# Performance work log

Hardware: AMD Instinct MI355X
Metric: run time of the kernel (lower is better)

Reference implementation:

```python
import jax, jax.numpy as jnp
import numpy as np

VS = VT = 32000; E = 512; H = 512; B = 32; S = 128; T = 128


def _gru_step(x, h, Wx, bx, Urz, brz, Un, bn):
    # x: [B, I], h: [B, H]
    gx = x @ Wx + bx                       # [B, 3H]
    xr, xz, xn = jnp.split(gx, 3, axis=-1)
    hrz = h @ Urz + brz                    # [B, 2H]
    hr, hz = jnp.split(hrz, 2, axis=-1)
    r = jax.nn.sigmoid(xr + hr)
    z = jax.nn.sigmoid(xz + hz)
    n = jnp.tanh(xn + (r * h) @ Un + bn)
    return (1.0 - z) * h + z * n


def setup_inputs() -> dict:
    key = jax.random.key(0)
    ks = jax.random.split(key, 24)
    s = 0.02
    f = lambda k, shape: (jax.random.normal(k, shape, dtype=jnp.float32) * s)
    return {
        "src": jax.random.randint(ks[0], (B, S), 0, VS),
        "tgt": jax.random.randint(ks[1], (B, T), 0, VT),
        "enc_embed": f(ks[2], (VS, E)),
        "enc_Wx": f(ks[3], (E, 3 * H)),
        "enc_bx": jnp.zeros((3 * H,), jnp.float32),
        "enc_Urz": f(ks[4], (H, 2 * H)),
        "enc_brz": jnp.zeros((2 * H,), jnp.float32),
        "enc_Un": f(ks[5], (H, H)),
        "enc_bn": jnp.zeros((H,), jnp.float32),
        "dec_embed": f(ks[6], (VT, E)),
        "dec_Wx": f(ks[7], (E + H, 3 * H)),
        "dec_bx": jnp.zeros((3 * H,), jnp.float32),
        "dec_Urz": f(ks[8], (H, 2 * H)),
        "dec_brz": jnp.zeros((2 * H,), jnp.float32),
        "dec_Un": f(ks[9], (H, H)),
        "dec_bn": jnp.zeros((H,), jnp.float32),
        "attn_Wh": f(ks[10], (H, H)),
        "attn_Ws": f(ks[11], (H, H)),
        "attn_v": f(ks[12], (H,)),
        "out_W": f(ks[13], (2 * H, VT)),
        "out_b": jnp.zeros((VT,), jnp.float32),
    }


def reference(src, tgt, enc_embed, enc_Wx, enc_bx, enc_Urz, enc_brz, enc_Un,
              enc_bn, dec_embed, dec_Wx, dec_bx, dec_Urz, dec_brz, dec_Un,
              dec_bn, attn_Wh, attn_Ws, attn_v, out_W, out_b):
    bs = src.shape[0]
    h0 = jnp.zeros((bs, H), dtype=enc_Wx.dtype)

    # -------- encoder: scan over src timesteps --------
    src_emb = enc_embed[src]                     # [B, S, E]

    def enc_step(h, x_t):
        h = _gru_step(x_t, h, enc_Wx, enc_bx, enc_Urz, enc_brz, enc_Un, enc_bn)
        return h, h

    h, enc_hs = jax.lax.scan(enc_step, h0, jnp.swapaxes(src_emb, 0, 1))
    enc_hs = jnp.swapaxes(enc_hs, 0, 1)          # [B, S, H]

    # precompute Wh(enc_hs), identical every decoder step
    wh_enc = enc_hs @ attn_Wh                    # [B, S, H]

    # -------- decoder: scan over tgt timesteps --------
    tgt_emb = dec_embed[tgt]                     # [B, T, E]

    def dec_step(h, emb_t):
        # Bahdanau attention
        energy = jnp.einsum('bsh,h->bs', jnp.tanh(wh_enc + (h @ attn_Ws)[:, None, :]), attn_v)
        attn = jax.nn.softmax(energy, axis=-1)   # [B, S]
        ctx = jnp.einsum('bs,bsh->bh', attn, enc_hs)
        x = jnp.concatenate([emb_t, ctx], axis=-1)   # [B, E+H]
        h = _gru_step(x, h, dec_Wx, dec_bx, dec_Urz, dec_brz, dec_Un, dec_bn)
        logits = jnp.concatenate([h, ctx], axis=-1) @ out_W + out_b
        out = jax.nn.log_softmax(logits, axis=-1)
        return h, out

    _, outputs = jax.lax.scan(dec_step, h, jnp.swapaxes(tgt_emb, 0, 1))
    return jnp.swapaxes(outputs, 0, 1)           # [B, T, VT]
```

## Files before the change

kernel.cpp:

```cpp
#include <hip/hip_runtime.h>
#include <stdint.h>

#define BATCH 32
#define SEQ   128
#define HID   512
#define VTOK  32000

typedef unsigned short u16;
typedef unsigned int   u32;
typedef unsigned long long u64;
typedef float    f32x4  __attribute__((ext_vector_type(4)));
typedef short    short8 __attribute__((ext_vector_type(8)));

__device__ __forceinline__ u16 f2bf(float f) {
    u32 u = __builtin_bit_cast(u32, f);
    return (u16)((u + 0x7FFFu + ((u >> 16) & 1u)) >> 16);
}
__device__ __forceinline__ float bf2f(u16 v) {
    u32 u = ((u32)v) << 16; return __builtin_bit_cast(float, u);
}
__device__ __forceinline__ float fexp2(float x) { return __builtin_amdgcn_exp2f(x); }
__device__ __forceinline__ float frcp(float x)  { return __builtin_amdgcn_rcpf(x); }
__device__ __forceinline__ float sigmoid_f(float x) {
    return frcp(1.f + fexp2(-1.442695040888963f * x));
}
__device__ __forceinline__ float tanh_f(float x) {
    return 1.f - 2.f * frcp(1.f + fexp2(2.885390081777927f * x));
}

__device__ __forceinline__ u32 ld_sc1_u32(const u32* p) {
    return __hip_atomic_load(p, __ATOMIC_RELAXED, __HIP_MEMORY_SCOPE_AGENT);
}
__device__ __forceinline__ void st_sc1_u32(u32* p, u32 v) {
    __hip_atomic_store(p, v, __ATOMIC_RELAXED, __HIP_MEMORY_SCOPE_AGENT);
}
__device__ __forceinline__ u64 ld_sc1_u64(const u64* p) {
    return __hip_atomic_load(p, __ATOMIC_RELAXED, __HIP_MEMORY_SCOPE_AGENT);
}
__device__ __forceinline__ short8 ldA(const u64* base) {
    union { u64 q[2]; short8 s; } u;
    u.q[0] = ld_sc1_u64(base);
    u.q[1] = ld_sc1_u64(base + 1);
    return u.s;
}

__device__ __forceinline__ void poll_ge(const u32* f, int idx, u32 gen) {
    const u32* p = f + (u32)idx * 16;
    while (ld_sc1_u32(p) < gen) {}
}
__device__ __forceinline__ void bump(u32* f, u32 gen) {
    asm volatile("s_waitcnt vmcnt(0)" ::: "memory");
    __syncthreads();
    if (threadIdx.x == 0) st_sc1_u32(f + (u32)blockIdx.x * 16, gen);
}


__global__ __launch_bounds__(256) void transpose_cvt(
    const float* __restrict__ src, u16* __restrict__ dst, int K, int N)
{
    __shared__ float tile[32][33];
    const int n0 = blockIdx.x * 32, k0 = blockIdx.y * 32;
    const int tx = threadIdx.x & 31, ty = threadIdx.x >> 5;
    #pragma unroll
    for (int j = 0; j < 32; j += 8)
        tile[ty + j][tx] = src[(size_t)(k0 + ty + j) * N + n0 + tx];
    __syncthreads();
    #pragma unroll
    for (int j = 0; j < 32; j += 8)
        dst[(size_t)(n0 + ty + j) * K + k0 + tx] = f2bf(tile[tx][ty + j]);
}

__global__ __launch_bounds__(256) void cvt_f32_bf16(
    const float* __restrict__ src, u16* __restrict__ dst)
{
    const size_t i = ((size_t)blockIdx.x * 256 + threadIdx.x) * 8;
    float4 v0 = *(const float4*)(src + i);
    float4 v1 = *(const float4*)(src + i + 4);
    uint4 pk;
    pk.x = (u32)f2bf(v0.x) | ((u32)f2bf(v0.y) << 16);
    pk.y = (u32)f2bf(v0.z) | ((u32)f2bf(v0.w) << 16);
    pk.z = (u32)f2bf(v1.x) | ((u32)f2bf(v1.y) << 16);
    pk.w = (u32)f2bf(v1.z) | ((u32)f2bf(v1.w) << 16);
    *(uint4*)(dst + i) = pk;
}

__global__ __launch_bounds__(128) void gather_emb_bf16(
    const int* __restrict__ idx, const float* __restrict__ emb, u16* __restrict__ out)
{
    const int r = blockIdx.x;
    const int token = idx[r];
    const int i = threadIdx.x * 4;
    float4 v = *(const float4*)(emb + (size_t)token * 512 + i);
    uint2 pk;
    pk.x = (u32)f2bf(v.x) | ((u32)f2bf(v.y) << 16);
    pk.y = (u32)f2bf(v.z) | ((u32)f2bf(v.w) << 16);
    *(uint2*)(out + (size_t)r * 512 + i) = pk;
}

__global__ __launch_bounds__(512) void init_state(u32* hg, u32* bar)
{
    const int i = blockIdx.x * 512 + threadIdx.x;
    hg[i] = 0u;
    if (blockIdx.x < 6) bar[blockIdx.x * 512 + threadIdx.x] = 0u;
}

__global__ __launch_bounds__(256) void gemm_bf16(
    const u16* __restrict__ A, const u16* __restrict__ BT,
    const float* __restrict__ bias, float* __restrict__ C,
    int M, int N, int K)
{
    __shared__ __align__(16) u16 As[128][40];
    __shared__ __align__(16) u16 Bs[128][40];
    const int tid  = threadIdx.x;
    const int lane = tid & 63, wave = tid >> 6;
    const int wm = (wave & 1) * 64, wn = (wave >> 1) * 64;
    const int lrow = lane & 15, lk = (lane >> 4) * 8;
    const int srow = tid >> 2, skof = (tid & 3) * 8;
    const size_t K_ = (size_t)K;
    const u16* Ag = A + ((size_t)blockIdx.y * 128 + srow) * K_ + skof;
    const u16* Bg = BT + ((size_t)blockIdx.x * 128 + srow) * K_ + skof;
    f32x4 acc[4][4] = {};
    for (int k0 = 0; k0 < K; k0 += 32) {
        uint4 a0 = *(const uint4*)(Ag + k0);
        uint4 a1 = *(const uint4*)(Ag + 64 * K_ + k0);
        uint4 b0 = *(const uint4*)(Bg + k0);
        uint4 b1 = *(const uint4*)(Bg + 64 * K_ + k0);
        __syncthreads();
        *(uint4*)&As[srow][skof]      = a0;
        *(uint4*)&As[srow + 64][skof] = a1;
        *(uint4*)&Bs[srow][skof]      = b0;
        *(uint4*)&Bs[srow + 64][skof] = b1;
        __syncthreads();
        short8 af[4], bf[4];
        #pragma unroll
        for (int i = 0; i < 4; ++i) af[i] = *(const short8*)&As[wm + i * 16 + lrow][lk];
        #pragma unroll
        for (int j = 0; j < 4; ++j) bf[j] = *(const short8*)&Bs[wn + j * 16 + lrow][lk];
        #pragma unroll
        for (int i = 0; i < 4; ++i)
            #pragma unroll
            for (int j = 0; j < 4; ++j)
                acc[i][j] = __builtin_amdgcn_mfma_f32_16x16x32_bf16(af[i], bf[j], acc[i][j], 0, 0, 0);
    }
    const int crow0 = blockIdx.y * 128 + wm + (lane >> 4) * 4;
    const int ccol0 = blockIdx.x * 128 + wn + (lane & 15);
    #pragma unroll
    for (int j = 0; j < 4; ++j) {
        const float bv = bias ? bias[ccol0 + j * 16] : 0.f;
        #pragma unroll
        for (int i = 0; i < 4; ++i)
            #pragma unroll
            for (int rr = 0; rr < 4; ++rr)
                C[(size_t)(crow0 + i * 16 + rr) * N + (ccol0 + j * 16)] = acc[i][j][rr] + bv;
    }
}

__global__ __launch_bounds__(512) void enc_coop(
    const float* __restrict__ gx, const u16* __restrict__ Urz, const u16* __restrict__ Un,
    const float* __restrict__ brz, const float* __restrict__ bn,
    u32* __restrict__ hg, u32* __restrict__ rhg, u32* __restrict__ zg,
    u16* __restrict__ enc_hs, u16* __restrict__ spack,
    u32* __restrict__ flags)
{
    const int w = blockIdx.x, tid = threadIdx.x;
    const int v = tid >> 6, lane = tid & 63;
    const int nl = lane & 15, kq = lane >> 4;
    const u64* rq = (const u64*)rhg;
    for (int t = 0; t < SEQ; ++t) {
        const u32* hgA = hg + (t & 1) * 8192;
        u32*       hgW = hg + ((t + 1) & 1) * 8192;
        const u64* hq  = (const u64*)hgA;
        { if (tid < 32) poll_ge(flags, tid, (u32)(2 * t)); __syncthreads(); }
        if (v < 2) {
            const int bt = v;
            const int n = w * 16 + nl;
            const int brow = bt * 16 + nl;
            float gxr_pf[4]; u32 hv_pf[4];
            #pragma unroll
            for (int rr = 0; rr < 4; ++rr) {
                const int b = bt * 16 + kq * 4 + rr;
                gxr_pf[rr] = gx[((size_t)(b * SEQ + t)) * 1536 + n];
                if (n < 512) hv_pf[rr] = ld_sc1_u32(hgA + b * 256 + (n >> 1));
            }
            const u16* wp = Urz + (size_t)n * 512 + kq * 8;
            f32x4 acc = {0.f, 0.f, 0.f, 0.f};
            #pragma unroll
            for (int k0 = 0; k0 < 512; k0 += 32) {
                short8 af = ldA(hq + brow * 128 + (k0 >> 2) + kq * 2);
                short8 bf = *(const short8*)(wp + k0);
                acc = __builtin_amdgcn_mfma_f32_16x16x32_bf16(af, bf, acc, 0, 0, 0);
            }
            if (n < 512) {
                u32 pk[4];
                #pragma unroll
                for (int rr = 0; rr < 4; ++rr) {
                    const float r = sigmoid_f(gxr_pf[rr] + acc[rr] + brz[n]);
                    const float hold = bf2f((u16)((n & 1) ? (hv_pf[rr] >> 16) : (hv_pf[rr] & 0xFFFF)));
                    pk[rr] = (u32)f2bf(r * hold);
                }
                #pragma unroll
                for (int rr = 0; rr < 4; ++rr) {
                    u32 oth = (u32)__shfl_xor((int)pk[rr], 1);
                    if ((n & 1) == 0) {
                        const int b = bt * 16 + kq * 4 + rr;
                        st_sc1_u32(rhg + b * 256 + (n >> 1), (pk[rr] & 0xFFFF) | (oth << 16));
                    }
                }
            } else {
                #pragma unroll
                for (int rr = 0; rr < 4; ++rr) {
                    const int b = bt * 16 + kq * 4 + rr;
                    const float z = sigmoid_f(gxr_pf[rr] + acc[rr] + brz[n]);
                    st_sc1_u32(zg + (n - 512) * 32 + b, __float_as_uint(z));
                }
            }
        }
        bump(flags, (u32)(2 * t + 1));
        if (w < 32) {
            { if (tid < 64) poll_ge(flags, tid, (u32)(2 * t + 1)); __syncthreads(); }
            if (v < 2) {
                const int bt = v;
                const int n = w * 16 + nl;
                const int brow = bt * 16 + nl;
                float gxr_pf[4]; u32 hv_pf[4], zv_pf[4];
                #pragma unroll
                for (int rr = 0; rr < 4; ++rr) {
                    const int b = bt * 16 + kq * 4 + rr;
                    gxr_pf[rr] = gx[((size_t)(b * SEQ + t)) * 1536 + 1024 + n];
                    hv_pf[rr] = ld_sc1_u32(hgA + b * 256 + (n >> 1));
                    zv_pf[rr] = ld_sc1_u32(zg + n * 32 + b);
                }
                const u16* wp = Un + (size_t)n * 512 + kq * 8;
                f32x4 acc = {0.f, 0.f, 0.f, 0.f};
                #pragma unroll
                for (int k0 = 0; k0 < 512; k0 += 32) {
                    short8 af = ldA(rq + brow * 128 + (k0 >> 2) + kq * 2);
                    short8 bf = *(const short8*)(wp + k0);
                    acc = __builtin_amdgcn_mfma_f32_16x16x32_bf16(af, bf, acc, 0, 0, 0);
                }
                u32 pk[4];
                #pragma unroll
                for (int rr = 0; rr < 4; ++rr) {
                    const int b = bt * 16 + kq * 4 + rr;
                    const float nn = tanh_f(gxr_pf[rr] + acc[rr] + bn[n]);
                    const float z = __uint_as_float(zv_pf[rr]);
                    const float hold = bf2f((u16)((n & 1) ? (hv_pf[rr] >> 16) : (hv_pf[rr] & 0xFFFF)));
                    const float hn = (1.f - z) * hold + z * nn;
                    const u16 hb = f2bf(hn);
                    pk[rr] = (u32)hb;
                    enc_hs[((size_t)(b * SEQ + t)) * 512 + n] = hb;
                    spack[(((size_t)b * 16 + (t >> 3)) * 512 + n) * 8 + (t & 7)] = hb;
                }
                #pragma unroll
                for (int rr = 0; rr < 4; ++rr) {
                    u32 oth = (u32)__shfl_xor((int)pk[rr], 1);
                    if ((n & 1) == 0) {
                        const int b = bt * 16 + kq * 4 + rr;
                        st_sc1_u32(hgW + b * 256 + (n >> 1), (pk[rr] & 0xFFFF) | (oth << 16));
                    }
                }
            }
        }
        bump(flags, (u32)(2 * t + 2));
    }
}

__global__ __launch_bounds__(512) void dec_coop(
    const float* __restrict__ gxe, const u16* __restrict__ wh_bf, const u16* __restrict__ spack,
    const float* __restrict__ attn_v, const float* __restrict__ brz, const float* __restrict__ bn,
    const u16* __restrict__ Urz, const u16* __restrict__ Ws,
    const u16* __restrict__ WxC, const u16* __restrict__ Un,
    u32* __restrict__ hg, u32* __restrict__ rhg, u32* __restrict__ ctxg,
    u32* __restrict__ zg, u32* __restrict__ gg, u32* __restrict__ aWsg,
    u16* __restrict__ hctx, u32* __restrict__ flags)
{
    const int w = blockIdx.x, tid = threadIdx.x;
    const int v = tid >> 6, lane = tid & 63;
    const int nl = lane & 15, kq = lane >> 4;
    __shared__ float hWsL[4 * 132], redE[512], attnL[128];
    __shared__ u16 ctxL[512];
    const u64* rq = (const u64*)rhg;
    const u64* cq = (const u64*)ctxg;
    for (int t = 0; t < SEQ; ++t) {
        const u32* hgA = hg + (t & 1) * 8192;
        u32*       hgW = hg + ((t + 1) & 1) * 8192;
        const u64* hq  = (const u64*)hgA;
        f32x4 aPk = {0.f, 0.f, 0.f, 0.f};
        { if (tid < 32) poll_ge(flags, tid, (u32)(4 * t)); __syncthreads(); }
        if (v < 2) {
            const int bt = v;
            const int n = w * 16 + nl;
            const int brow = bt * 16 + nl;
            const u16* wp = (n < 1024 ? Urz + (size_t)n * 512
                                      : Ws + (size_t)(n - 1024) * 512) + kq * 8;
            f32x4 acc = {0.f, 0.f, 0.f, 0.f};
            #pragma unroll
            for (int k0 = 0; k0 < 512; k0 += 32) {
                short8 af = ldA(hq + brow * 128 + (k0 >> 2) + kq * 2);
                short8 bf = *(const short8*)(wp + k0);
                acc = __builtin_amdgcn_mfma_f32_16x16x32_bf16(af, bf, acc, 0, 0, 0);
            }
            if (n < 1024) {
                aPk = acc;
            } else {
                #pragma unroll
                for (int rr = 0; rr < 4; ++rr) {
                    const int b = bt * 16 + kq * 4 + rr;
                    st_sc1_u32(aWsg + (n - 1024) * 32 + b, __float_as_uint(acc[rr]));
                }
            }
        }
        bump(flags, (u32)(4 * t + 1));
        if (w < 32) {
            {
                const int l = tid;
                if (l < 96) {
                    int g0 = 4 * t - 1; if (g0 < 0) g0 = 0;
                    u32 g = (l >= 64) ? (u32)(4 * t + 1) : (u32)g0;
                    poll_ge(flags, l, g);
                }
                __syncthreads();
            }
            const int b = w;
            hWsL[(tid >> 7) * 132 + (tid & 127)] = __uint_as_float(ld_sc1_u32(aWsg + tid * 32 + b));
            __syncthreads();
            {
                const int s = tid >> 2, q = tid & 3;
                const u16* whr = wh_bf + ((size_t)(b * SEQ + s)) * 512 + q * 128;
                const float* avq = attn_v + q * 128;
                const float* hwq = &hWsL[q * 132];
                float e = 0.f;
                #pragma unroll 4
                for (int i = 0; i < 128; i += 8) {
                    uint4 wv = *(const uint4*)(whr + i);
                    float4 h0 = *(const float4*)(hwq + i);
                    float4 h1 = *(const float4*)(hwq + i + 4);
                    float4 v0 = *(const float4*)(avq + i);
                    float4 v1 = *(const float4*)(avq + i + 4);
                    e += v0.x * tanh_f(bf2f((u16)(wv.x & 0xFFFF)) + h0.x)
                       + v0.y * tanh_f(bf2f((u16)(wv.x >> 16))    + h0.y)
                       + v0.z * tanh_f(bf2f((u16)(wv.y & 0xFFFF)) + h0.z)
                       + v0.w * tanh_f(bf2f((u16)(wv.y >> 16))    + h0.w)
                       + v1.x * tanh_f(bf2f((u16)(wv.z & 0xFFFF)) + h1.x)
                       + v1.y * tanh_f(bf2f((u16)(wv.z >> 16))    + h1.y)
                       + v1.z * tanh_f(bf2f((u16)(wv.w & 0xFFFF)) + h1.z)
                       + v1.w * tanh_f(bf2f((u16)(wv.w >> 16))    + h1.w);
                }
                redE[tid] = e;
            }
            __syncthreads();
            if (tid < 64) {
                float e0 = redE[4 * tid] + redE[4 * tid + 1] + redE[4 * tid + 2] + redE[4 * tid + 3];
                float e1 = redE[4 * (tid + 64)] + redE[4 * (tid + 64) + 1]
                         + redE[4 * (tid + 64) + 2] + redE[4 * (tid + 64) + 3];
                float m = fmaxf(e0, e1);
                for (int o = 32; o >= 1; o >>= 1) m = fmaxf(m, __shfl_xor(m, o));
                float p0 = fexp2((e0 - m) * 1.442695040888963f);
                float p1 = fexp2((e1 - m) * 1.442695040888963f);
                float ss = p0 + p1;
                for (int o = 32; o >= 1; o >>= 1) ss += __shfl_xor(ss, o);
                const float inv = frcp(ss);
                attnL[tid]      = p0 * inv;
                attnL[tid + 64] = p1 * inv;
            }
            __syncthreads();
            {
                const int d = tid;
                float cv = 0.f;
                const u16* sp = spack + ((size_t)b * 16 * 512 + d) * 8;
                #pragma unroll 4
                for (int sb = 0; sb < 16; ++sb) {
                    uint4 sv = *(const uint4*)(sp + (size_t)sb * 4096);
                    const float* al = &attnL[sb * 8];
                    cv += al[0] * bf2f((u16)(sv.x & 0xFFFF)) + al[1] * bf2f((u16)(sv.x >> 16))
                        + al[2] * bf2f((u16)(sv.y & 0xFFFF)) + al[3] * bf2f((u16)(sv.y >> 16))
                        + al[4] * bf2f((u16)(sv.z & 0xFFFF)) + al[5] * bf2f((u16)(sv.z >> 16))
                        + al[6] * bf2f((u16)(sv.w & 0xFFFF)) + al[7] * bf2f((u16)(sv.w >> 16));
                }
                const u16 cb = f2bf(cv);
                ctxL[d] = cb;
                hctx[((size_t)(b * SEQ + t)) * 1024 + 512 + d] = cb;
            }
            __syncthreads();
            if (tid < 256) {
                u32 pk = (u32)ctxL[2 * tid] | ((u32)ctxL[2 * tid + 1] << 16);
                st_sc1_u32(ctxg + b * 256 + tid, pk);
            }
        }
        bump(flags, (u32)(4 * t + 2));
        { if (tid < 32) poll_ge(flags, tid, (u32)(4 * t + 2)); __syncthreads(); }
        if (v < 2) {
            const int bt = v;
            const int n = w * 16 + nl;
            const int brow = bt * 16 + nl;
            float gxr_pf[4]; u32 hv_pf[4];
            #pragma unroll
            for (int rr = 0; rr < 4; ++rr) {
                const int b = bt * 16 + kq * 4 + rr;
                gxr_pf[rr] = gxe[((size_t)(b * SEQ + t)) * 1536 + n];
                if (n < 512) hv_pf[rr] = ld_sc1_u32(hgA + b * 256 + (n >> 1));
            }
            const u16* wp = WxC + (size_t)n * 512 + kq * 8;
            f32x4 acc = {0.f, 0.f, 0.f, 0.f};
            #pragma unroll
            for (int k0 = 0; k0 < 512; k0 += 32) {
                short8 af = ldA(cq + brow * 128 + (k0 >> 2) + kq * 2);
                short8 bf = *(const short8*)(wp + k0);
                acc = __builtin_amdgcn_mfma_f32_16x16x32_bf16(af, bf, acc, 0, 0, 0);
            }
            if (n < 512) {
                u32 pk[4];
                #pragma unroll
                for (int rr = 0; rr < 4; ++rr) {
                    const float r = sigmoid_f(gxr_pf[rr] + acc[rr] + aPk[rr] + brz[n]);
                    const float hold = bf2f((u16)((n & 1) ? (hv_pf[rr] >> 16) : (hv_pf[rr] & 0xFFFF)));
                    pk[rr] = (u32)f2bf(r * hold);
                }
                #pragma unroll
                for (int rr = 0; rr < 4; ++rr) {
                    u32 oth = (u32)__shfl_xor((int)pk[rr], 1);
                    if ((n & 1) == 0) {
                        const int b = bt * 16 + kq * 4 + rr;
                        st_sc1_u32(rhg + b * 256 + (n >> 1), (pk[rr] & 0xFFFF) | (oth << 16));
                    }
                }
            } else if (n < 1024) {
                #pragma unroll
                for (int rr = 0; rr < 4; ++rr) {
                    const int b = bt * 16 + kq * 4 + rr;
                    const float z = sigmoid_f(gxr_pf[rr] + acc[rr] + aPk[rr] + brz[n]);
                    st_sc1_u32(zg + (n - 512) * 32 + b, __float_as_uint(z));
                }
            } else {
                #pragma unroll
                for (int rr = 0; rr < 4; ++rr) {
                    const int b = bt * 16 + kq * 4 + rr;
                    st_sc1_u32(gg + (n - 1024) * 32 + b, __float_as_uint(gxr_pf[rr] + acc[rr]));
                }
            }
        }
        bump(flags, (u32)(4 * t + 3));
        if (w < 32) {
            {
                const int l = tid;
                if (l < 32) poll_ge(flags, l, (u32)(4 * t + 3));
                else if (l == 32) poll_ge(flags, 32 + w, (u32)(4 * t + 3));
                else if (l == 33) poll_ge(flags, 64 + w, (u32)(4 * t + 3));
                __syncthreads();
            }
            if (v < 2) {
                const int bt = v;
                const int n = w * 16 + nl;
                const int brow = bt * 16 + nl;
                u32 gv_pf[4], zv_pf[4], hv_pf[4];
                #pragma unroll
                for (int rr = 0; rr < 4; ++rr) {
                    const int b = bt * 16 + kq * 4 + rr;
                    gv_pf[rr] = ld_sc1_u32(gg + n * 32 + b);
                    zv_pf[rr] = ld_sc1_u32(zg + n * 32 + b);
                    hv_pf[rr] = ld_sc1_u32(hgA + b * 256 + (n >> 1));
                }
                const u16* wp = Un + (size_t)n * 512 + kq * 8;
                f32x4 acc = {0.f, 0.f, 0.f, 0.f};
                #pragma unroll
                for (int k0 = 0; k0 < 512; k0 += 32) {
                    short8 af = ldA(rq + brow * 128 + (k0 >> 2) + kq * 2);
                    short8 bf = *(const short8*)(wp + k0);
                    acc = __builtin_amdgcn_mfma_f32_16x16x32_bf16(af, bf, acc, 0, 0, 0);
                }
                u32 pk[4];
                #pragma unroll
                for (int rr = 0; rr < 4; ++rr) {
                    const int b = bt * 16 + kq * 4 + rr;
                    const float nn = tanh_f(__uint_as_float(gv_pf[rr]) + acc[rr] + bn[n]);
                    const float z = __uint_as_float(zv_pf[rr]);
                    const float hold = bf2f((u16)((n & 1) ? (hv_pf[rr] >> 16) : (hv_pf[rr] & 0xFFFF)));
                    const float hn = (1.f - z) * hold + z * nn;
                    const u16 hb = f2bf(hn);
                    pk[rr] = (u32)hb;
                    hctx[((size_t)(b * SEQ + t)) * 1024 + n] = hb;
                }
                #pragma unroll
                for (int rr = 0; rr < 4; ++rr) {
                    u32 oth = (u32)__shfl_xor((int)pk[rr], 1);
                    if ((n & 1) == 0) {
                        const int b = bt * 16 + kq * 4 + rr;
                        st_sc1_u32(hgW + b * 256 + (n >> 1), (pk[rr] & 0xFFFF) | (oth << 16));
                    }
                }
            }
        }
        bump(flags, (u32)(4 * t + 4));
    }
}

__global__ __launch_bounds__(256) void log_softmax_rows(float* __restrict__ out)
{
    const int row = blockIdx.x, tid = threadIdx.x;
    float* p = out + (size_t)row * VTOK;
    __shared__ float rbM[4], rbS[4];
    const float L2E = 1.442695040888963f;
    float m = -3.0e38f, s = 0.f;
    for (int i = tid * 4; i < VTOK; i += 1024) {
        float4 v = *(const float4*)(p + i);
        float lm = fmaxf(fmaxf(v.x, v.y), fmaxf(v.z, v.w));
        float nm = fmaxf(m, lm);
        s = s * fexp2((m - nm) * L2E)
          + fexp2((v.x - nm) * L2E) + fexp2((v.y - nm) * L2E)
          + fexp2((v.z - nm) * L2E) + fexp2((v.w - nm) * L2E);
        m = nm;
    }
    for (int o = 32; o >= 1; o >>= 1) {
        float om = __shfl_xor(m, o), os = __shfl_xor(s, o);
        float nm = fmaxf(m, om);
        s = s * fexp2((m - nm) * L2E) + os * fexp2((om - nm) * L2E);
        m = nm;
    }
    if ((tid & 63) == 0) { rbM[tid >> 6] = m; rbS[tid >> 6] = s; }
    __syncthreads();
    {
        float fm = fmaxf(fmaxf(rbM[0], rbM[1]), fmaxf(rbM[2], rbM[3]));
        float fs = rbS[0] * fexp2((rbM[0] - fm) * L2E) + rbS[1] * fexp2((rbM[1] - fm) * L2E)
                 + rbS[2] * fexp2((rbM[2] - fm) * L2E) + rbS[3] * fexp2((rbM[3] - fm) * L2E);
        m = fm; s = fs;
    }
    const float lse = m + __builtin_amdgcn_logf(s) * 0.6931471805599453f;
    for (int i = tid * 4; i < VTOK; i += 1024) {
        float4 v = *(const float4*)(p + i);
        v.x -= lse; v.y -= lse; v.z -= lse; v.w -= lse;
        *(float4*)(p + i) = v;
    }
}

extern "C" void kernel_launch(void* const* d_in, const int* in_sizes, int n_in,
                              void* d_out, int out_size, void* d_ws, size_t ws_size,
                              hipStream_t stream)
{
    (void)in_sizes; (void)n_in; (void)out_size; (void)ws_size;
    const int*   src       = (const int*)  d_in[0];
    const int*   tgt       = (const int*)  d_in[1];
    const float* enc_embed = (const float*)d_in[2];
    const float* enc_Wx    = (const float*)d_in[3];
    const float* enc_bx    = (const float*)d_in[4];
    const float* enc_Urz   = (const float*)d_in[5];
    const float* enc_brz   = (const float*)d_in[6];
    const float* enc_Un    = (const float*)d_in[7];
    const float* enc_bn    = (const float*)d_in[8];
    const float* dec_embed = (const float*)d_in[9];
    const float* dec_Wx    = (const float*)d_in[10];
    const float* dec_bx    = (const float*)d_in[11];
    const float* dec_Urz   = (const float*)d_in[12];
    const float* dec_brz   = (const float*)d_in[13];
    const float* dec_Un    = (const float*)d_in[14];
    const float* dec_bn    = (const float*)d_in[15];
    const float* attn_Wh   = (const float*)d_in[16];
    const float* attn_Ws   = (const float*)d_in[17];
    const float* attn_v    = (const float*)d_in[18];
    const float* out_W     = (const float*)d_in[19];
    const float* out_b     = (const float*)d_in[20];

    char* ob = (char*)d_out;
    float* gx_enc   = (float*)(ob + 0);
    float* gxe_dec  = (float*)(ob + 25165824);
    float* wh_enc   = (float*)(ob + 50331648);
    u16*   Aenc     = (u16*)(ob + 58720256);
    u16*   Adec     = (u16*)(ob + 62914560);
    u16*   enc_hs   = (u16*)(ob + 67108864);
    u16*   spack    = (u16*)(ob + 71303168);
    u16*   wh_bf    = (u16*)(ob + 75497472);
    u16*   encWxT   = (u16*)(ob + 79691776);
    u16*   decWxET  = (u16*)(ob + 81264640);
    u16*   WhT      = (u16*)(ob + 82837504);
    u16*   UrzET    = (u16*)(ob + 83361792);
    u16*   UnET     = (u16*)(ob + 84410368);
    u16*   UrzDT    = (u16*)(ob + 84934656);
    u16*   UnDT     = (u16*)(ob + 85983232);
    u16*   WsT      = (u16*)(ob + 86507520);
    u16*   WxCT     = (u16*)(ob + 87031808);
    u32*   hg       = (u32*)(ob + 88604672);
    u32*   rhg      = (u32*)(ob + 88670208);
    u32*   ctxg     = (u32*)(ob + 88702976);
    u32*   zg       = (u32*)(ob + 88735744);
    u32*   gg       = (u32*)(ob + 88801280);
    u32*   aWsg     = (u32*)(ob + 88866816);
    u32*   barp     = (u32*)(ob + 88932352);

    char* wb = (char*)d_ws;
    u16* outWT = (u16*)(wb + 0);
    u16* hctx  = (u16*)(wb + 65536000);

    transpose_cvt<<<dim3(48, 16),   256, 0, stream>>>(enc_Wx,  encWxT, 512, 1536);
    transpose_cvt<<<dim3(48, 16),   256, 0, stream>>>(dec_Wx,  decWxET,512, 1536);
    transpose_cvt<<<dim3(16, 16),   256, 0, stream>>>(attn_Wh, WhT,    512, 512);
    transpose_cvt<<<dim3(1000, 32), 256, 0, stream>>>(out_W,   outWT, 1024, 32000);
    transpose_cvt<<<dim3(32, 16),   256, 0, stream>>>(enc_Urz, UrzET,  512, 1024);
    transpose_cvt<<<dim3(16, 16),   256, 0, stream>>>(enc_Un,  UnET,   512, 512);
    transpose_cvt<<<dim3(32, 16),   256, 0, stream>>>(dec_Urz, UrzDT,  512, 1024);
    transpose_cvt<<<dim3(16, 16),   256, 0, stream>>>(dec_Un,  UnDT,   512, 512);
    transpose_cvt<<<dim3(16, 16),   256, 0, stream>>>(attn_Ws, WsT,    512, 512);
    transpose_cvt<<<dim3(48, 16),   256, 0, stream>>>(dec_Wx + (size_t)512 * 1536, WxCT, 512, 1536);
    gather_emb_bf16<<<4096, 128, 0, stream>>>(src, enc_embed, Aenc);
    gather_emb_bf16<<<4096, 128, 0, stream>>>(tgt, dec_embed, Adec);

    gemm_bf16<<<dim3(12, 32), 256, 0, stream>>>(Aenc, encWxT,  enc_bx, gx_enc,  4096, 1536, 512);
    gemm_bf16<<<dim3(12, 32), 256, 0, stream>>>(Adec, decWxET, dec_bx, gxe_dec, 4096, 1536, 512);

    init_state<<<32, 512, 0, stream>>>(hg, barp);

    {
        u32* encF = barp;
        void* args[] = { (void*)&gx_enc, (void*)&UrzET, (void*)&UnET, (void*)&enc_brz,
                         (void*)&enc_bn, (void*)&hg, (void*)&rhg, (void*)&zg,
                         (void*)&enc_hs, (void*)&spack, (void*)&encF };
        hipLaunchCooperativeKernel((void*)enc_coop, dim3(64), dim3(512), args, 0, stream);
    }

    gemm_bf16<<<dim3(4, 32), 256, 0, stream>>>(enc_hs, WhT, nullptr, wh_enc, 4096, 512, 512);
    cvt_f32_bf16<<<1024, 256, 0, stream>>>(wh_enc, wh_bf);

    {
        u32* decF = barp + 1536;
        void* args[] = { (void*)&gxe_dec, (void*)&wh_bf, (void*)&spack, (void*)&attn_v,
                         (void*)&dec_brz, (void*)&dec_bn, (void*)&UrzDT, (void*)&WsT,
                         (void*)&WxCT, (void*)&UnDT, (void*)&hg, (void*)&rhg, (void*)&ctxg,
                         (void*)&zg, (void*)&gg, (void*)&aWsg, (void*)&hctx, (void*)&decF };
        hipLaunchCooperativeKernel((void*)dec_coop, dim3(96), dim3(512), args, 0, stream);
    }

    gemm_bf16<<<dim3(250, 32), 256, 0, stream>>>(hctx, outWT, out_b, (float*)d_out, 4096, VTOK, 1024);
    log_softmax_rows<<<4096, 256, 0, stream>>>((float*)d_out);
}
```

Measured before the change: 6.397 ms.

## Shrink cooperative GRU kernels to 32 blocks with LDS-resident weights

The encoder and decoder persistent kernels drop from 64 and 96 blocks to 32 blocks. Each block now loads its slice of recurrent weights (Urz, Un, Ws, WxC) into shared memory once before the time loop, instead of re-reading them from global memory every step. The per-phase flag polling is replaced by a uniform 32-block all-to-all barrier. Fewer blocks means cheaper barriers and less flag traffic, at the cost of more waves of work per block, larger LDS use (about 150KB in the decoder), and less parallelism in each phase.

```diff
diff --git a/kernel.cpp b/kernel.cpp
--- a/kernel.cpp
+++ b/kernel.cpp
@@ -44,14 +44,15 @@
     return u.s;
 }
 
-__device__ __forceinline__ void poll_ge(const u32* f, int idx, u32 gen) {
-    const u32* p = f + (u32)idx * 16;
-    while (ld_sc1_u32(p) < gen) {}
-}
-__device__ __forceinline__ void bump(u32* f, u32 gen) {
+__device__ __forceinline__ void gbar32(u32* flags, u32 gen) {
     asm volatile("s_waitcnt vmcnt(0)" ::: "memory");
     __syncthreads();
-    if (threadIdx.x == 0) st_sc1_u32(f + (u32)blockIdx.x * 16, gen);
+    if (threadIdx.x == 0) st_sc1_u32(flags + (u32)blockIdx.x * 16, gen);
+    const int i = threadIdx.x;
+    if (i < 32 && i != (int)blockIdx.x) {
+        while (ld_sc1_u32(flags + i * 16) < gen) {}
+    }
+    __syncthreads();
 }
 
 
@@ -101,7 +102,7 @@
 {
     const int i = blockIdx.x * 512 + threadIdx.x;
     hg[i] = 0u;
-    if (blockIdx.x < 6) bar[blockIdx.x * 512 + threadIdx.x] = 0u;
+    if (blockIdx.x < 2) bar[blockIdx.x * 512 + threadIdx.x] = 0u;
 }
 
 __global__ __launch_bounds__(256) void gemm_bf16(
@@ -165,15 +166,25 @@
     const int w = blockIdx.x, tid = threadIdx.x;
     const int v = tid >> 6, lane = tid & 63;
     const int nl = lane & 15, kq = lane >> 4;
+    __shared__ __align__(16) u16 UrzS[32][520];
+    __shared__ __align__(16) u16 UnS[16][520];
+    for (int idx = tid; idx < 32 * 64; idx += 512) {
+        const int r = idx >> 6, c = idx & 63;
+        *(uint4*)&UrzS[r][c * 8] = *(const uint4*)(Urz + (size_t)(w * 32 + r) * 512 + c * 8);
+    }
+    for (int idx = tid; idx < 16 * 64; idx += 512) {
+        const int r = idx >> 6, c = idx & 63;
+        *(uint4*)&UnS[r][c * 8] = *(const uint4*)(Un + (size_t)(w * 16 + r) * 512 + c * 8);
+    }
+    __syncthreads();
     const u64* rq = (const u64*)rhg;
     for (int t = 0; t < SEQ; ++t) {
         const u32* hgA = hg + (t & 1) * 8192;
         u32*       hgW = hg + ((t + 1) & 1) * 8192;
         const u64* hq  = (const u64*)hgA;
-        { if (tid < 32) poll_ge(flags, tid, (u32)(2 * t)); __syncthreads(); }
-        if (v < 2) {
-            const int bt = v;
-            const int n = w * 16 + nl;
+        if (v < 4) {
+            const int bt = v & 1, tl = v >> 1;
+            const int n = w * 32 + tl * 16 + nl;
             const int brow = bt * 16 + nl;
             float gxr_pf[4]; u32 hv_pf[4];
             #pragma unroll
@@ -182,12 +193,12 @@
                 gxr_pf[rr] = gx[((size_t)(b * SEQ + t)) * 1536 + n];
                 if (n < 512) hv_pf[rr] = ld_sc1_u32(hgA + b * 256 + (n >> 1));
             }
-            const u16* wp = Urz + (size_t)n * 512 + kq * 8;
+            const u16* wl = &UrzS[tl * 16 + nl][0];
             f32x4 acc = {0.f, 0.f, 0.f, 0.f};
             #pragma unroll
             for (int k0 = 0; k0 < 512; k0 += 32) {
                 short8 af = ldA(hq + brow * 128 + (k0 >> 2) + kq * 2);
-                short8 bf = *(const short8*)(wp + k0);
+                short8 bf = *(const short8*)(wl + k0 + kq * 8);
                 acc = __builtin_amdgcn_mfma_f32_16x16x32_bf16(af, bf, acc, 0, 0, 0);
             }
             if (n < 512) {
@@ -215,53 +226,50 @@
                 }
             }
         }
-        bump(flags, (u32)(2 * t + 1));
-        if (w < 32) {
-            { if (tid < 64) poll_ge(flags, tid, (u32)(2 * t + 1)); __syncthreads(); }
-            if (v < 2) {
-                const int bt = v;
-                const int n = w * 16 + nl;
-                const int brow = bt * 16 + nl;
-                float gxr_pf[4]; u32 hv_pf[4], zv_pf[4];
-                #pragma unroll
-                for (int rr = 0; rr < 4; ++rr) {
+        gbar32(flags, (u32)(2 * t + 1));
+        if (v < 2) {
+            const int bt = v;
+            const int n = w * 16 + nl;
+            const int brow = bt * 16 + nl;
+            float gxr_pf[4]; u32 hv_pf[4], zv_pf[4];
+            #pragma unroll
+            for (int rr = 0; rr < 4; ++rr) {
+                const int b = bt * 16 + kq * 4 + rr;
+                gxr_pf[rr] = gx[((size_t)(b * SEQ + t)) * 1536 + 1024 + n];
+                hv_pf[rr] = ld_sc1_u32(hgA + b * 256 + (n >> 1));
+                zv_pf[rr] = ld_sc1_u32(zg + n * 32 + b);
+            }
+            const u16* wl = &UnS[nl][0];
+            f32x4 acc = {0.f, 0.f, 0.f, 0.f};
+            #pragma unroll
+            for (int k0 = 0; k0 < 512; k0 += 32) {
+                short8 af = ldA(rq + brow * 128 + (k0 >> 2) + kq * 2);
+                short8 bf = *(const short8*)(wl + k0 + kq * 8);
+                acc = __builtin_amdgcn_mfma_f32_16x16x32_bf16(af, bf, acc, 0, 0, 0);
+            }
+            u32 pk[4];
+            #pragma unroll
+            for (int rr = 0; rr < 4; ++rr) {
+                const int b = bt * 16 + kq * 4 + rr;
+                const float nn = tanh_f(gxr_pf[rr] + acc[rr] + bn[n]);
+                const float z = __uint_as_float(zv_pf[rr]);
+                const float hold = bf2f((u16)((n & 1) ? (hv_pf[rr] >> 16) : (hv_pf[rr] & 0xFFFF)));
+                const float hn = (1.f - z) * hold + z * nn;
+                const u16 hb = f2bf(hn);
+                pk[rr] = (u32)hb;
+                enc_hs[((size_t)(b * SEQ + t)) * 512 + n] = hb;
+                spack[(((size_t)b * 16 + (t >> 3)) * 512 + n) * 8 + (t & 7)] = hb;
+            }
+            #pragma unroll
+            for (int rr = 0; rr < 4; ++rr) {
+                u32 oth = (u32)__shfl_xor((int)pk[rr], 1);
+                if ((n & 1) == 0) {
                     const int b = bt * 16 + kq * 4 + rr;
-                    gxr_pf[rr] = gx[((size_t)(b * SEQ + t)) * 1536 + 1024 + n];
-                    hv_pf[rr] = ld_sc1_u32(hgA + b * 256 + (n >> 1));
-                    zv_pf[rr] = ld_sc1_u32(zg + n * 32 + b);
-                }
-                const u16* wp = Un + (size_t)n * 512 + kq * 8;
-                f32x4 acc = {0.f, 0.f, 0.f, 0.f};
-                #pragma unroll
-                for (int k0 = 0; k0 < 512; k0 += 32) {
-                    short8 af = ldA(rq + brow * 128 + (k0 >> 2) + kq * 2);
-                    short8 bf = *(const short8*)(wp + k0);
-                    acc = __builtin_amdgcn_mfma_f32_16x16x32_bf16(af, bf, acc, 0, 0, 0);
-                }
-                u32 pk[4];
-                #pragma unroll
-                for (int rr = 0; rr < 4; ++rr) {
-                    const int b = bt * 16 + kq * 4 + rr;
-                    const float nn = tanh_f(gxr_pf[rr] + acc[rr] + bn[n]);
-                    const float z = __uint_as_float(zv_pf[rr]);
-                    const float hold = bf2f((u16)((n & 1) ? (hv_pf[rr] >> 16) : (hv_pf[rr] & 0xFFFF)));
-                    const float hn = (1.f - z) * hold + z * nn;
-                    const u16 hb = f2bf(hn);
-                    pk[rr] = (u32)hb;
-                    enc_hs[((size_t)(b * SEQ + t)) * 512 + n] = hb;
-                    spack[(((size_t)b * 16 + (t >> 3)) * 512 + n) * 8 + (t & 7)] = hb;
-                }
-                #pragma unroll
-                for (int rr = 0; rr < 4; ++rr) {
-                    u32 oth = (u32)__shfl_xor((int)pk[rr], 1);
-                    if ((n & 1) == 0) {
-                        const int b = bt * 16 + kq * 4 + rr;
-                        st_sc1_u32(hgW + b * 256 + (n >> 1), (pk[rr] & 0xFFFF) | (oth << 16));
-                    }
+                    st_sc1_u32(hgW + b * 256 + (n >> 1), (pk[rr] & 0xFFFF) | (oth << 16));
                 }
             }
         }
-        bump(flags, (u32)(2 * t + 2));
+        gbar32(flags, (u32)(2 * t + 2));
     }
 }
 
@@ -277,8 +285,24 @@
     const int w = blockIdx.x, tid = threadIdx.x;
     const int v = tid >> 6, lane = tid & 63;
     const int nl = lane & 15, kq = lane >> 4;
+    __shared__ __align__(16) u16 UWsS[48][520];
+    __shared__ __align__(16) u16 WxCS[48][520];
+    __shared__ __align__(16) u16 UnS2[16][520];
     __shared__ float hWsL[4 * 132], redE[512], attnL[128];
     __shared__ u16 ctxL[512];
+    for (int idx = tid; idx < 48 * 64; idx += 512) {
+        const int r = idx >> 6, c = idx & 63;
+        const int gcol = w * 48 + r;
+        const u16* s0 = (gcol < 1024 ? Urz + (size_t)gcol * 512
+                                     : Ws + (size_t)(gcol - 1024) * 512) + c * 8;
+        *(uint4*)&UWsS[r][c * 8] = *(const uint4*)s0;
+        *(uint4*)&WxCS[r][c * 8] = *(const uint4*)(WxC + (size_t)gcol * 512 + c * 8);
+    }
+    for (int idx = tid; idx < 16 * 64; idx += 512) {
+        const int r = idx >> 6, c = idx & 63;
+        *(uint4*)&UnS2[r][c * 8] = *(const uint4*)(Un + (size_t)(w * 16 + r) * 512 + c * 8);
+    }
+    __syncthreads();
     const u64* rq = (const u64*)rhg;
     const u64* cq = (const u64*)ctxg;
     for (int t = 0; t < SEQ; ++t) {
@@ -286,18 +310,16 @@
         u32*       hgW = hg + ((t + 1) & 1) * 8192;
         const u64* hq  = (const u64*)hgA;
         f32x4 aPk = {0.f, 0.f, 0.f, 0.f};
-        { if (tid < 32) poll_ge(flags, tid, (u32)(4 * t)); __syncthreads(); }
-        if (v < 2) {
-            const int bt = v;
-            const int n = w * 16 + nl;
+        if (v < 6) {
+            const int bt = v & 1, tl = v >> 1;
+            const int n = w * 48 + tl * 16 + nl;
             const int brow = bt * 16 + nl;
-            const u16* wp = (n < 1024 ? Urz + (size_t)n * 512
-                                      : Ws + (size_t)(n - 1024) * 512) + kq * 8;
+            const u16* wl = &UWsS[tl * 16 + nl][0];
             f32x4 acc = {0.f, 0.f, 0.f, 0.f};
             #pragma unroll
             for (int k0 = 0; k0 < 512; k0 += 32) {
                 short8 af = ldA(hq + brow * 128 + (k0 >> 2) + kq * 2);
-                short8 bf = *(const short8*)(wp + k0);
+                short8 bf = *(const short8*)(wl + k0 + kq * 8);
                 acc = __builtin_amdgcn_mfma_f32_16x16x32_bf16(af, bf, acc, 0, 0, 0);
             }
             if (n < 1024) {
@@ -310,17 +332,8 @@
                 }
             }
         }
-        bump(flags, (u32)(4 * t + 1));
-        if (w < 32) {
-            {
-                const int l = tid;
-                if (l < 96) {
-                    int g0 = 4 * t - 1; if (g0 < 0) g0 = 0;
-                    u32 g = (l >= 64) ? (u32)(4 * t + 1) : (u32)g0;
-                    poll_ge(flags, l, g);
-                }
-                __syncthreads();
-            }
+        gbar32(flags, (u32)(4 * t + 1));
+        {
             const int b = w;
             hWsL[(tid >> 7) * 132 + (tid & 127)] = __uint_as_float(ld_sc1_u32(aWsg + tid * 32 + b));
             __syncthreads();
@@ -387,11 +400,10 @@
                 st_sc1_u32(ctxg + b * 256 + tid, pk);
             }
         }
-        bump(flags, (u32)(4 * t + 2));
-        { if (tid < 32) poll_ge(flags, tid, (u32)(4 * t + 2)); __syncthreads(); }
-        if (v < 2) {
-            const int bt = v;
-            const int n = w * 16 + nl;
+        gbar32(flags, (u32)(4 * t + 2));
+        if (v < 6) {
+            const int bt = v & 1, tl = v >> 1;
+            const int n = w * 48 + tl * 16 + nl;
             const int brow = bt * 16 + nl;
             float gxr_pf[4]; u32 hv_pf[4];
             #pragma unroll
@@ -400,12 +412,12 @@
                 gxr_pf[rr] = gxe[((size_t)(b * SEQ + t)) * 1536 + n];
                 if (n < 512) hv_pf[rr] = ld_sc1_u32(hgA + b * 256 + (n >> 1));
             }
-            const u16* wp = WxC + (size_t)n * 512 + kq * 8;
+            const u16* wl = &WxCS[tl * 16 + nl][0];
             f32x4 acc = {0.f, 0.f, 0.f, 0.f};
             #pragma unroll
             for (int k0 = 0; k0 < 512; k0 += 32) {
                 short8 af = ldA(cq + brow * 128 + (k0 >> 2) + kq * 2);
-                short8 bf = *(const short8*)(wp + k0);
+                short8 bf = *(const short8*)(wl + k0 + kq * 8);
                 acc = __builtin_amdgcn_mfma_f32_16x16x32_bf16(af, bf, acc, 0, 0, 0);
             }
             if (n < 512) {
@@ -439,58 +451,49 @@
                 }
             }
         }
-        bump(flags, (u32)(4 * t + 3));
-        if (w < 32) {
-            {
-                const int l = tid;
-                if (l < 32) poll_ge(flags, l, (u32)(4 * t + 3));
-                else if (l == 32) poll_ge(flags, 32 + w, (u32)(4 * t + 3));
-                else if (l == 33) poll_ge(flags, 64 + w, (u32)(4 * t + 3));
-                __syncthreads();
-            }
-            if (v < 2) {
-                const int bt = v;
-                const int n = w * 16 + nl;
-                const int brow = bt * 16 + nl;
-                u32 gv_pf[4], zv_pf[4], hv_pf[4];
-                #pragma unroll
-                for (int rr = 0; rr < 4; ++rr) {
+        gbar32(flags, (u32)(4 * t + 3));
+        if (v < 2) {
+            const int bt = v;
+            const int n = w * 16 + nl;
+            const int brow = bt * 16 + nl;
+            u32 gv_pf[4], zv_pf[4], hv_pf[4];
+            #pragma unroll
+            for (int rr = 0; rr < 4; ++rr) {
+                const int b = bt * 16 + kq * 4 + rr;
+                gv_pf[rr] = ld_sc1_u32(gg + n * 32 + b);
+                zv_pf[rr] = ld_sc1_u32(zg + n * 32 + b);
+                hv_pf[rr] = ld_sc1_u32(hgA + b * 256 + (n >> 1));
+            }
+            const u16* wl = &UnS2[nl][0];
+            f32x4 acc = {0.f, 0.f, 0.f, 0.f};
+            #pragma unroll
+            for (int k0 = 0; k0 < 512; k0 += 32) {
+                short8 af = ldA(rq + brow * 128 + (k0 >> 2) + kq * 2);
+                short8 bf = *(const short8*)(wl + k0 + kq * 8);
+                acc = __builtin_amdgcn_mfma_f32_16x16x32_bf16(af, bf, acc, 0, 0, 0);
+            }
+            u32 pk[4];
+            #pragma unroll
+            for (int rr = 0; rr < 4; ++rr) {
+                const int b = bt * 16 + kq * 4 + rr;
+                const float nn = tanh_f(__uint_as_float(gv_pf[rr]) + acc[rr] + bn[n]);
+                const float z = __uint_as_float(zv_pf[rr]);
+                const float hold = bf2f((u16)((n & 1) ? (hv_pf[rr] >> 16) : (hv_pf[rr] & 0xFFFF)));
+                const float hn = (1.f - z) * hold + z * nn;
+                const u16 hb = f2bf(hn);
+                pk[rr] = (u32)hb;
+                hctx[((size_t)(b * SEQ + t)) * 1024 + n] = hb;
+            }
+            #pragma unroll
+            for (int rr = 0; rr < 4; ++rr) {
+                u32 oth = (u32)__shfl_xor((int)pk[rr], 1);
+                if ((n & 1) == 0) {
                     const int b = bt * 16 + kq * 4 + rr;
-                    gv_pf[rr] = ld_sc1_u32(gg + n * 32 + b);
-                    zv_pf[rr] = ld_sc1_u32(zg + n * 32 + b);
-                    hv_pf[rr] = ld_sc1_u32(hgA + b * 256 + (n >> 1));
-                }
-                const u16* wp = Un + (size_t)n * 512 + kq * 8;
-                f32x4 acc = {0.f, 0.f, 0.f, 0.f};
-                #pragma unroll
-                for (int k0 = 0; k0 < 512; k0 += 32) {
-                    short8 af = ldA(rq + brow * 128 + (k0 >> 2) + kq * 2);
-                    short8 bf = *(const short8*)(wp + k0);
-                    acc = __builtin_amdgcn_mfma_f32_16x16x32_bf16(af, bf, acc, 0, 0, 0);
-                }
-                u32 pk[4];
-                #pragma unroll
-                for (int rr = 0; rr < 4; ++rr) {
-                    const int b = bt * 16 + kq * 4 + rr;
-                    const float nn = tanh_f(__uint_as_float(gv_pf[rr]) + acc[rr] + bn[n]);
-                    const float z = __uint_as_float(zv_pf[rr]);
-                    const float hold = bf2f((u16)((n & 1) ? (hv_pf[rr] >> 16) : (hv_pf[rr] & 0xFFFF)));
-                    const float hn = (1.f - z) * hold + z * nn;
-                    const u16 hb = f2bf(hn);
-                    pk[rr] = (u32)hb;
-                    hctx[((size_t)(b * SEQ + t)) * 1024 + n] = hb;
-                }
-                #pragma unroll
-                for (int rr = 0; rr < 4; ++rr) {
-                    u32 oth = (u32)__shfl_xor((int)pk[rr], 1);
-                    if ((n & 1) == 0) {
-                        const int b = bt * 16 + kq * 4 + rr;
-                        st_sc1_u32(hgW + b * 256 + (n >> 1), (pk[rr] & 0xFFFF) | (oth << 16));
-                    }
+                    st_sc1_u32(hgW + b * 256 + (n >> 1), (pk[rr] & 0xFFFF) | (oth << 16));
                 }
             }
         }
-        bump(flags, (u32)(4 * t + 4));
+        gbar32(flags, (u32)(4 * t + 4));
     }
 }
 
@@ -612,19 +615,19 @@
         void* args[] = { (void*)&gx_enc, (void*)&UrzET, (void*)&UnET, (void*)&enc_brz,
                          (void*)&enc_bn, (void*)&hg, (void*)&rhg, (void*)&zg,
                          (void*)&enc_hs, (void*)&spack, (void*)&encF };
-        hipLaunchCooperativeKernel((void*)enc_coop, dim3(64), dim3(512), args, 0, stream);
+        hipLaunchCooperativeKernel((void*)enc_coop, dim3(32), dim3(512), args, 0, stream);
     }
 
     gemm_bf16<<<dim3(4, 32), 256, 0, stream>>>(enc_hs, WhT, nullptr, wh_enc, 4096, 512, 512);
     cvt_f32_bf16<<<1024, 256, 0, stream>>>(wh_enc, wh_bf);
 
     {
-        u32* decF = barp + 1536;
+        u32* decF = barp + 512;
         void* args[] = { (void*)&gxe_dec, (void*)&wh_bf, (void*)&spack, (void*)&attn_v,
                          (void*)&dec_brz, (void*)&dec_bn, (void*)&UrzDT, (void*)&WsT,
                          (void*)&WxCT, (void*)&UnDT, (void*)&hg, (void*)&rhg, (void*)&ctxg,
                          (void*)&zg, (void*)&gg, (void*)&aWsg, (void*)&hctx, (void*)&decF };
-        hipLaunchCooperativeKernel((void*)dec_coop, dim3(96), dim3(512), args, 0, stream);
+        hipLaunchCooperativeKernel((void*)dec_coop, dim3(32), dim3(512), args, 0, stream);
     }
 
     gemm_bf16<<<dim3(250, 32), 256, 0, stream>>>(hctx, outWT, out_b, (float*)d_out, 4096, VTOK, 1024);
```

Result: slower. 6.725 ms (+5.1%).
